# Optimization experiments

Hardware: AMD Instinct MI355X
Metric: run time of the kernel (lower is better)

## Reference

```python
import jax, jax.numpy as jnp
import numpy as np

EPS = 1e-8
VOX_WIDTH = 1.0
CURV_THRESH = 0.5


def _build_kernels():
    """Nine 3x3x3 central finite-difference stencils, pre-divided by vox_width / vox_width^2."""
    def zk():
        return np.zeros((3, 3, 3), np.float32)
    ks = {}
    # first derivatives (central difference), denominator vox_width
    for name, ax in (('ddx', 0), ('ddy', 1), ('ddz', 2)):
        k = zk(); i = [1, 1, 1]
        i[ax] = 0; k[tuple(i)] = -0.5
        i[ax] = 2; k[tuple(i)] = 0.5
        ks[name] = k / VOX_WIDTH
    # pure second derivatives, denominator vox_width^2
    for name, ax in (('d2dx2', 0), ('d2dy2', 1), ('d2dz2', 2)):
        k = zk(); i = [1, 1, 1]
        i[ax] = 0; k[tuple(i)] = 1.0
        i[ax] = 1; k[tuple(i)] = -2.0
        i[ax] = 2; k[tuple(i)] = 1.0
        ks[name] = k / VOX_WIDTH ** 2
    # mixed second derivatives, denominator vox_width^2
    for name, (a, b) in (('d2dxdy', (0, 1)), ('d2dxdz', (0, 2)), ('d2dydz', (1, 2))):
        k = zk()
        for sa, sb, v in ((0, 0, 0.25), (0, 2, -0.25), (2, 0, -0.25), (2, 2, 0.25)):
            i = [1, 1, 1]; i[a] = sa; i[b] = sb; k[tuple(i)] = v
        ks[name] = k / VOX_WIDTH ** 2
    order = ['ddx', 'ddy', 'ddz', 'd2dx2', 'd2dy2', 'd2dz2', 'd2dxdy', 'd2dxdz', 'd2dydz']
    return np.stack([ks[n] for n in order])[:, None]  # [9, 1, 3, 3, 3]


_KERNELS = jnp.asarray(_build_kernels())


def setup_inputs() -> dict:
    key = jax.random.key(0)
    phi = jax.random.normal(key, (2, 1, 192, 192, 192), dtype=jnp.float32)
    return {"phi": phi}


def reference(phi):
    # all nine stencils as one valid 3D conv: [N, 9, D-2, H-2, W-2]
    g = jax.lax.conv_general_dilated(
        phi, _KERNELS, window_strides=(1, 1, 1), padding='VALID',
        dimension_numbers=('NCDHW', 'OIDHW', 'NCDHW'))
    gx, gy, gz, hxx, hyy, hzz, hxy, hxz, hyz = (g[:, i:i + 1] for i in range(9))

    mag = jnp.sqrt(gx * gx + gy * gy + gz * gz + EPS)
    mag3 = mag ** 3

    # mean curvature: sum_{i!=j} g_i^2 H_jj - 2 sum_{i<j} g_i g_j H_ij, over |grad|^3
    cross = gx * gy * hxy + gx * gz * hxz + gy * gz * hyz
    mean_c = (gx * gx * (hyy + hzz) + gy * gy * (hxx + hzz) + gz * gz * (hxx + hyy)
              - 2.0 * cross) / (mag3 + EPS)

    # gaussian curvature: laplacian/|grad| - (g^T H g)/|grad|^3
    lap = (hxx + hyy + hzz) / (mag + EPS)
    quad = (gx * gx * hxx + gy * gy * hyy + gz * gz * hzz + 2.0 * cross) / (mag3 + EPS)
    gauss = lap - quad

    k1 = mean_c + jnp.sqrt(jnp.abs(mean_c ** 2 - gauss) + EPS)
    pen = jax.nn.relu((k1 / (CURV_THRESH + EPS)) ** 2 - 1.0)

    # zero crossings of phi over 3x3x3 neighborhoods (valid -> matches conv output shape)
    mn = jax.lax.reduce_window(phi, jnp.inf, jax.lax.min, (1, 1, 3, 3, 3), (1, 1, 1, 1, 1), 'VALID')
    mx = jax.lax.reduce_window(phi, -jnp.inf, jax.lax.max, (1, 1, 3, 3, 3), (1, 1, 1, 1, 1), 'VALID')
    phi_zero = jax.lax.stop_gradient((mn * mx < 0).astype(phi.dtype))

    return jnp.sum(phi_zero * pen) / (jnp.sum(phi_zero) + EPS)
```

## Files before the change

### kernel.cpp

```cpp
#include <hip/hip_runtime.h>


typedef float v2f __attribute__((ext_vector_type(2)));

constexpr int DIM  = 192;
constexpr int ODIM = 190;
constexpr int TX = 32, TY = 32, CZ = 19;
constexpr int NTX = 6, NTY = 6, NTZ = 10;
constexpr int PLANE = DIM * DIM;
constexpr int NBLOCKS = 2 * NTZ * NTY * NTX;

struct Row { v2f A, B, C; };
struct Slice {
    Row   r[3];
    float xmn[4], xmx[4];
};

#define PREF(T4, T2, g) do {                                             \
    const float* base_ = pn + (zbase + (g)) * PLANE;                     \
    _Pragma("unroll")                                                    \
    for (int dy = 0; dy < 3; ++dy) {                                     \
        T4[dy] = *(const float4*)(base_ + yoff[dy] + c4);                \
        T2[dy] = *(const float2*)(base_ + yoff[dy] + c2);                \
    } } while (0)

#define UNPACK(S, T4, T2) do {                                           \
    float mn6[6], mx6[6];                                                \
    _Pragma("unroll")                                                    \
    for (int dy = 0; dy < 3; ++dy) {                                     \
        const float4 a = T4[dy]; const float2 b = T2[dy];                \
        (S).r[dy].A = (v2f){a.x, a.z};                                   \
        (S).r[dy].B = (v2f){a.y, a.w};                                   \
        (S).r[dy].C = (v2f){b.x, b.y};                                   \
        if (dy == 0) {                                                   \
            mn6[0] = a.x; mn6[1] = a.y; mn6[2] = a.z;                    \
            mn6[3] = a.w; mn6[4] = b.x; mn6[5] = b.y;                    \
            mx6[0] = a.x; mx6[1] = a.y; mx6[2] = a.z;                    \
            mx6[3] = a.w; mx6[4] = b.x; mx6[5] = b.y;                    \
        } else {                                                         \
            mn6[0] = fminf(mn6[0], a.x); mx6[0] = fmaxf(mx6[0], a.x);    \
            mn6[1] = fminf(mn6[1], a.y); mx6[1] = fmaxf(mx6[1], a.y);    \
            mn6[2] = fminf(mn6[2], a.z); mx6[2] = fmaxf(mx6[2], a.z);    \
            mn6[3] = fminf(mn6[3], a.w); mx6[3] = fmaxf(mx6[3], a.w);    \
            mn6[4] = fminf(mn6[4], b.x); mx6[4] = fmaxf(mx6[4], b.x);    \
            mn6[5] = fminf(mn6[5], b.y); mx6[5] = fmaxf(mx6[5], b.y);    \
        }                                                                \
    }                                                                    \
    _Pragma("unroll")                                                    \
    for (int j = 0; j < 4; ++j) {                                        \
        (S).xmn[j] = fminf(fminf(mn6[j], mn6[j + 1]), mn6[j + 2]);       \
        (S).xmx[j] = fmaxf(fmaxf(mx6[j], mx6[j + 1]), mx6[j + 2]);       \
    } } while (0)

__global__ __launch_bounds__(256, 3) void curv_main(const float* __restrict__ phi,
                                                    double* __restrict__ acc,
                                                    float* __restrict__ out,
                                                    unsigned* __restrict__ ticket,
                                                    int mode) {
    int bx = blockIdx.x;
    const int tx = bx % NTX; bx /= NTX;
    const int ty = bx % NTY; bx /= NTY;
    const int tz = bx % NTZ; bx /= NTZ;
    const int n  = bx;

    const int xbase = tx * TX, ybase = ty * TY, zbase = tz * CZ;
    const int tid = threadIdx.x;
    const int row = tid >> 3;
    const int x0  = (tid & 7) * 4;
    const float* pn = phi + (long long)n * DIM * PLANE;

    const int c4 = xbase + x0;
    int c2t = c4 + 4; if (c2t > DIM - 2) c2t = DIM - 2;
    const int c2 = c2t;
    int yoff[3];
#pragma unroll
    for (int dy = 0; dy < 3; ++dy) {
        int iy = ybase + row + dy; if (iy > DIM - 1) iy = DIM - 1;
        yoff[dy] = iy * DIM;
    }

    float4 tA4[3]; float2 tA2[3];
    float4 tB4[3]; float2 tB2[3];

    float fsp = 0.0f, fsc = 0.0f;
    const float EPSF = 1e-8f;
    const float EPS4 = 4e-8f;
    const int oy = ybase + row;

    bool vmask[4];
#pragma unroll
    for (int j = 0; j < 4; ++j)
        vmask[j] = (oy < ODIM) && (xbase + x0 + j < ODIM);

    auto PK = [](const Row& w, int k) -> v2f {
        return k == 0 ? w.A
             : (k == 1 ? w.B
             : (k == 2 ? (v2f){w.A.y, w.C.x}
                       : (v2f){w.B.y, w.C.y}));
    };

    auto compute = [&](const Slice& s0, const Slice& s1, const Slice& s2) {
        float wmn[4], wmx[4];
#pragma unroll
        for (int j = 0; j < 4; ++j) {
            wmn[j] = fminf(fminf(s0.xmn[j], s1.xmn[j]), s2.xmn[j]);
            wmx[j] = fmaxf(fmaxf(s0.xmx[j], s1.xmx[j]), s2.xmx[j]);
        }

#pragma unroll
        for (int p = 0; p < 2; ++p) {
            const v2f a0 = PK(s0.r[1], p + 1);
            const v2f a2 = PK(s2.r[1], p + 1);
            const v2f b0 = PK(s1.r[0], p + 1);
            const v2f b2 = PK(s1.r[2], p + 1);
            const v2f cc = PK(s1.r[1], p + 1);
            const v2f zm = PK(s1.r[1], p);
            const v2f zp = PK(s1.r[1], p + 2);

            v2f Gx = a2 - a0;
            v2f Gy = b2 - b0;
            v2f Gz = zp - zm;

            v2f c2v = 2.0f * cc;
            v2f hxx = a0 - c2v + a2;
            v2f hyy = b0 - c2v + b2;
            v2f hzz = zm - c2v + zp;

            v2f Mxy = PK(s0.r[0], p + 1) - PK(s0.r[2], p + 1)
                    - PK(s2.r[0], p + 1) + PK(s2.r[2], p + 1);
            v2f Mxz = PK(s0.r[1], p) - PK(s0.r[1], p + 2)
                    - PK(s2.r[1], p) + PK(s2.r[1], p + 2);
            v2f Myz = PK(s1.r[0], p) - PK(s1.r[0], p + 2)
                    - PK(s1.r[2], p) + PK(s1.r[2], p + 2);

            v2f Gx2 = Gx * Gx, Gy2 = Gy * Gy, Gz2 = Gz * Gz;
            v2f mag2G = Gx2 + Gy2 + Gz2 + EPS4;

            v2f r = (v2f){ __builtin_amdgcn_rsqf(mag2G.x),
                           __builtin_amdgcn_rsqf(mag2G.y) };
            v2f r3 = r * r * r;
            v2f twor3 = r3 + r3;

            v2f crossG = Gx * Gy * Mxy + Gx * Gz * Mxz + Gy * Gz * Myz;

            v2f num1 = Gx2 * (hyy + hzz) + Gy2 * (hxx + hzz) +
                       Gz2 * (hxx + hyy) - 0.5f * crossG;
            v2f mean_c = num1 * twor3;
            v2f lap   = (hxx + hyy + hzz) * (r + r);
            v2f num2  = Gx2 * hxx + Gy2 * hyy + Gz2 * hzz + 0.5f * crossG;
            v2f quad  = num2 * twor3;
            v2f gauss = lap - quad;

            v2f disc = mean_c * mean_c - gauss;
            v2f sq = (v2f){ sqrtf(fabsf(disc.x) + EPSF),
                            sqrtf(fabsf(disc.y) + EPSF) };
            v2f k1 = mean_c + sq;
            v2f t  = 2.0f * k1;
            v2f pen2 = t * t - 1.0f;

#pragma unroll
            for (int e = 0; e < 2; ++e) {
                const int j = p + 2 * e;
                float pen = fmaxf(e ? pen2.y : pen2.x, 0.0f);
                if (vmask[j] && (wmn[j] * wmx[j] < 0.0f)) {
                    fsp += pen;
                    fsc += 1.0f;
                }
            }
        }
    };

    Slice s0, s1, s2;

    PREF(tA4, tA2, 0); PREF(tB4, tB2, 1);
    UNPACK(s0, tA4, tA2); PREF(tA4, tA2, 2);
    UNPACK(s1, tB4, tB2); PREF(tB4, tB2, 3);

    UNPACK(s2, tA4, tA2); PREF(tA4, tA2, 4);  compute(s0, s1, s2);
    UNPACK(s0, tB4, tB2); PREF(tB4, tB2, 5);  compute(s1, s2, s0);
    UNPACK(s1, tA4, tA2); PREF(tA4, tA2, 6);  compute(s2, s0, s1);
    UNPACK(s2, tB4, tB2); PREF(tB4, tB2, 7);  compute(s0, s1, s2);
    UNPACK(s0, tA4, tA2); PREF(tA4, tA2, 8);  compute(s1, s2, s0);
    UNPACK(s1, tB4, tB2); PREF(tB4, tB2, 9);  compute(s2, s0, s1);
    UNPACK(s2, tA4, tA2); PREF(tA4, tA2, 10); compute(s0, s1, s2);
    UNPACK(s0, tB4, tB2); PREF(tB4, tB2, 11); compute(s1, s2, s0);
    UNPACK(s1, tA4, tA2); PREF(tA4, tA2, 12); compute(s2, s0, s1);
    UNPACK(s2, tB4, tB2); PREF(tB4, tB2, 13); compute(s0, s1, s2);
    UNPACK(s0, tA4, tA2); PREF(tA4, tA2, 14); compute(s1, s2, s0);
    UNPACK(s1, tB4, tB2); PREF(tB4, tB2, 15); compute(s2, s0, s1);
    UNPACK(s2, tA4, tA2); PREF(tA4, tA2, 16); compute(s0, s1, s2);
    UNPACK(s0, tB4, tB2); PREF(tB4, tB2, 17); compute(s1, s2, s0);
    UNPACK(s1, tA4, tA2); PREF(tA4, tA2, 18); compute(s2, s0, s1);
    UNPACK(s2, tB4, tB2); PREF(tB4, tB2, 19); compute(s0, s1, s2);
    UNPACK(s0, tA4, tA2); PREF(tA4, tA2, 20); compute(s1, s2, s0);
    UNPACK(s1, tB4, tB2);                     compute(s2, s0, s1);
    UNPACK(s2, tA4, tA2);                     compute(s0, s1, s2);

    double sp = (double)fsp, sc = (double)fsc;
#pragma unroll
    for (int off = 32; off > 0; off >>= 1) {
        sp += __shfl_down(sp, off, 64);
        sc += __shfl_down(sc, off, 64);
    }

    __shared__ double lsp[4], lsc[4];
    __shared__ int is_last;
    const int wave = tid >> 6, lane = tid & 63;
    if (lane == 0) { lsp[wave] = sp; lsc[wave] = sc; }
    __syncthreads();
    if (tid == 0) {
        double tp = lsp[0] + lsp[1] + lsp[2] + lsp[3];
        double tc = lsc[0] + lsc[1] + lsc[2] + lsc[3];
        if (mode) {
            acc[2 * blockIdx.x]     = tp;
            acc[2 * blockIdx.x + 1] = tc;
            __threadfence();
            unsigned prev = atomicAdd(ticket, 1u);
            is_last = (prev == (unsigned)(NBLOCKS - 1)) ? 1 : 0;
        } else {
            atomicAdd(&acc[0], tp);
            atomicAdd(&acc[1], tc);
            is_last = 0;
        }
    }
    __syncthreads();

    if (is_last) {
        __threadfence();
        double rp = 0.0, rc = 0.0;
        for (int i = tid; i < NBLOCKS; i += 256) {
            rp += acc[2 * i];
            rc += acc[2 * i + 1];
        }
#pragma unroll
        for (int off = 32; off > 0; off >>= 1) {
            rp += __shfl_down(rp, off, 64);
            rc += __shfl_down(rc, off, 64);
        }
        if (lane == 0) { lsp[wave] = rp; lsc[wave] = rc; }
        __syncthreads();
        if (tid == 0) {
            double tp = lsp[0] + lsp[1] + lsp[2] + lsp[3];
            double tc = lsc[0] + lsc[1] + lsc[2] + lsc[3];
            out[0] = (float)(tp / (tc + 1e-8));
        }
    }
}

__global__ void curv_reduce(const double* __restrict__ acc,
                            float* __restrict__ out) {
    if (threadIdx.x == 0)
        out[0] = (float)(acc[0] / (acc[1] + 1e-8));
}

extern "C" void kernel_launch(void* const* d_in, const int* in_sizes, int n_in,
                              void* d_out, int out_size, void* d_ws, size_t ws_size,
                              hipStream_t stream) {
    const float* phi = (const float*)d_in[0];
    float* out = (float*)d_out;
    double* acc = (double*)d_ws;

    const size_t need = (size_t)(2 * NBLOCKS) * sizeof(double) + sizeof(unsigned);
    if (ws_size >= need) {
        unsigned* ticket = (unsigned*)(acc + 2 * NBLOCKS);
        hipMemsetAsync(ticket, 0, sizeof(unsigned), stream);
        curv_main<<<NBLOCKS, 256, 0, stream>>>(phi, acc, out, ticket, 1);
    } else {
        hipMemsetAsync(d_ws, 0, 2 * sizeof(double), stream);
        curv_main<<<NBLOCKS, 256, 0, stream>>>(phi, acc, out, (unsigned*)nullptr, 0);
        curv_reduce<<<1, 256, 0, stream>>>(acc, out);
    }
}
```

Measured before the change: 121.7 us.

## Precompute shifted pair vectors and replace last-block ticket reduction with a separate reduce kernel

Each slice now stores four pre-packed v2f windows per row, including the two shifted pairs, so the stencil code indexes them directly instead of building them per use. The fused last-block reduction, with its ticket memset, atomic ticket and thread fences, is replaced by plain per-block partial writes followed by a separate one-block reduce kernel. This removes the memset and the fence/atomic tail from the main kernel, at the cost of an extra kernel launch and slightly more register state per slice.

```diff
diff --git a/kernel.cpp b/kernel.cpp
--- a/kernel.cpp
+++ b/kernel.cpp
@@ -10,9 +10,8 @@
 constexpr int PLANE = DIM * DIM;
 constexpr int NBLOCKS = 2 * NTZ * NTY * NTX;
 
-struct Row { v2f A, B, C; };
 struct Slice {
-    Row   r[3];
+    v2f   q[3][4];
     float xmn[4], xmx[4];
 };
 
@@ -29,9 +28,10 @@
     _Pragma("unroll")                                                    \
     for (int dy = 0; dy < 3; ++dy) {                                     \
         const float4 a = T4[dy]; const float2 b = T2[dy];                \
-        (S).r[dy].A = (v2f){a.x, a.z};                                   \
-        (S).r[dy].B = (v2f){a.y, a.w};                                   \
-        (S).r[dy].C = (v2f){b.x, b.y};                                   \
+        (S).q[dy][0] = (v2f){a.x, a.z};                                  \
+        (S).q[dy][1] = (v2f){a.y, a.w};                                  \
+        (S).q[dy][2] = (v2f){a.z, b.x};                                  \
+        (S).q[dy][3] = (v2f){a.w, b.y};                                  \
         if (dy == 0) {                                                   \
             mn6[0] = a.x; mn6[1] = a.y; mn6[2] = a.z;                    \
             mn6[3] = a.w; mn6[4] = b.x; mn6[5] = b.y;                    \
@@ -54,9 +54,7 @@
 
 __global__ __launch_bounds__(256, 3) void curv_main(const float* __restrict__ phi,
                                                     double* __restrict__ acc,
-                                                    float* __restrict__ out,
-                                                    unsigned* __restrict__ ticket,
-                                                    int mode) {
+                                                    int use_partials) {
     int bx = blockIdx.x;
     const int tx = bx % NTX; bx /= NTX;
     const int ty = bx % NTY; bx /= NTY;
@@ -92,13 +90,6 @@
     for (int j = 0; j < 4; ++j)
         vmask[j] = (oy < ODIM) && (xbase + x0 + j < ODIM);
 
-    auto PK = [](const Row& w, int k) -> v2f {
-        return k == 0 ? w.A
-             : (k == 1 ? w.B
-             : (k == 2 ? (v2f){w.A.y, w.C.x}
-                       : (v2f){w.B.y, w.C.y}));
-    };
-
     auto compute = [&](const Slice& s0, const Slice& s1, const Slice& s2) {
         float wmn[4], wmx[4];
 #pragma unroll
@@ -109,29 +100,21 @@
 
 #pragma unroll
         for (int p = 0; p < 2; ++p) {
-            const v2f a0 = PK(s0.r[1], p + 1);
-            const v2f a2 = PK(s2.r[1], p + 1);
-            const v2f b0 = PK(s1.r[0], p + 1);
-            const v2f b2 = PK(s1.r[2], p + 1);
-            const v2f cc = PK(s1.r[1], p + 1);
-            const v2f zm = PK(s1.r[1], p);
-            const v2f zp = PK(s1.r[1], p + 2);
-
-            v2f Gx = a2 - a0;
-            v2f Gy = b2 - b0;
-            v2f Gz = zp - zm;
-
-            v2f c2v = 2.0f * cc;
-            v2f hxx = a0 - c2v + a2;
-            v2f hyy = b0 - c2v + b2;
-            v2f hzz = zm - c2v + zp;
-
-            v2f Mxy = PK(s0.r[0], p + 1) - PK(s0.r[2], p + 1)
-                    - PK(s2.r[0], p + 1) + PK(s2.r[2], p + 1);
-            v2f Mxz = PK(s0.r[1], p) - PK(s0.r[1], p + 2)
-                    - PK(s2.r[1], p) + PK(s2.r[1], p + 2);
-            v2f Myz = PK(s1.r[0], p) - PK(s1.r[0], p + 2)
-                    - PK(s1.r[2], p) + PK(s1.r[2], p + 2);
+            v2f Gx = s2.q[1][p + 1] - s0.q[1][p + 1];
+            v2f Gy = s1.q[2][p + 1] - s1.q[0][p + 1];
+            v2f Gz = s1.q[1][p + 2] - s1.q[1][p];
+
+            v2f c2v = 2.0f * s1.q[1][p + 1];
+            v2f hxx = s0.q[1][p + 1] - c2v + s2.q[1][p + 1];
+            v2f hyy = s1.q[0][p + 1] - c2v + s1.q[2][p + 1];
+            v2f hzz = s1.q[1][p] - c2v + s1.q[1][p + 2];
+
+            v2f Mxy = s0.q[0][p + 1] - s0.q[2][p + 1]
+                    - s2.q[0][p + 1] + s2.q[2][p + 1];
+            v2f Mxz = s0.q[1][p] - s0.q[1][p + 2]
+                    - s2.q[1][p] + s2.q[1][p + 2];
+            v2f Myz = s1.q[0][p] - s1.q[0][p + 2]
+                    - s1.q[2][p] + s1.q[2][p + 2];
 
             v2f Gx2 = Gx * Gx, Gy2 = Gy * Gy, Gz2 = Gz * Gz;
             v2f mag2G = Gx2 + Gy2 + Gz2 + EPS4;
@@ -204,53 +187,48 @@
     }
 
     __shared__ double lsp[4], lsc[4];
-    __shared__ int is_last;
     const int wave = tid >> 6, lane = tid & 63;
     if (lane == 0) { lsp[wave] = sp; lsc[wave] = sc; }
     __syncthreads();
     if (tid == 0) {
         double tp = lsp[0] + lsp[1] + lsp[2] + lsp[3];
         double tc = lsc[0] + lsc[1] + lsc[2] + lsc[3];
-        if (mode) {
+        if (use_partials) {
             acc[2 * blockIdx.x]     = tp;
             acc[2 * blockIdx.x + 1] = tc;
-            __threadfence();
-            unsigned prev = atomicAdd(ticket, 1u);
-            is_last = (prev == (unsigned)(NBLOCKS - 1)) ? 1 : 0;
         } else {
             atomicAdd(&acc[0], tp);
             atomicAdd(&acc[1], tc);
-            is_last = 0;
-        }
-    }
+        }
+    }
+}
+
+__global__ __launch_bounds__(256) void curv_reduce(const double* __restrict__ part,
+                                                   int nblocks, int use_partials,
+                                                   float* __restrict__ out) {
+    double sp = 0.0, sc = 0.0;
+    if (use_partials) {
+        for (int i = threadIdx.x; i < nblocks; i += 256) {
+            sp += part[2 * i];
+            sc += part[2 * i + 1];
+        }
+    } else if (threadIdx.x == 0) {
+        sp = part[0]; sc = part[1];
+    }
+#pragma unroll
+    for (int off = 32; off > 0; off >>= 1) {
+        sp += __shfl_down(sp, off, 64);
+        sc += __shfl_down(sc, off, 64);
+    }
+    __shared__ double lsp[4], lsc[4];
+    const int wave = threadIdx.x >> 6, lane = threadIdx.x & 63;
+    if (lane == 0) { lsp[wave] = sp; lsc[wave] = sc; }
     __syncthreads();
-
-    if (is_last) {
-        __threadfence();
-        double rp = 0.0, rc = 0.0;
-        for (int i = tid; i < NBLOCKS; i += 256) {
-            rp += acc[2 * i];
-            rc += acc[2 * i + 1];
-        }
-#pragma unroll
-        for (int off = 32; off > 0; off >>= 1) {
-            rp += __shfl_down(rp, off, 64);
-            rc += __shfl_down(rc, off, 64);
-        }
-        if (lane == 0) { lsp[wave] = rp; lsc[wave] = rc; }
-        __syncthreads();
-        if (tid == 0) {
-            double tp = lsp[0] + lsp[1] + lsp[2] + lsp[3];
-            double tc = lsc[0] + lsc[1] + lsc[2] + lsc[3];
-            out[0] = (float)(tp / (tc + 1e-8));
-        }
-    }
-}
-
-__global__ void curv_reduce(const double* __restrict__ acc,
-                            float* __restrict__ out) {
-    if (threadIdx.x == 0)
-        out[0] = (float)(acc[0] / (acc[1] + 1e-8));
+    if (threadIdx.x == 0) {
+        double tp = lsp[0] + lsp[1] + lsp[2] + lsp[3];
+        double tc = lsc[0] + lsc[1] + lsc[2] + lsc[3];
+        out[0] = (float)(tp / (tc + 1e-8));
+    }
 }
 
 extern "C" void kernel_launch(void* const* d_in, const int* in_sizes, int n_in,
@@ -260,14 +238,11 @@
     float* out = (float*)d_out;
     double* acc = (double*)d_ws;
 
-    const size_t need = (size_t)(2 * NBLOCKS) * sizeof(double) + sizeof(unsigned);
-    if (ws_size >= need) {
-        unsigned* ticket = (unsigned*)(acc + 2 * NBLOCKS);
-        hipMemsetAsync(ticket, 0, sizeof(unsigned), stream);
-        curv_main<<<NBLOCKS, 256, 0, stream>>>(phi, acc, out, ticket, 1);
-    } else {
+    const int use_partials = (ws_size >= (size_t)(2 * NBLOCKS) * sizeof(double)) ? 1 : 0;
+    if (!use_partials) {
         hipMemsetAsync(d_ws, 0, 2 * sizeof(double), stream);
-        curv_main<<<NBLOCKS, 256, 0, stream>>>(phi, acc, out, (unsigned*)nullptr, 0);
-        curv_reduce<<<1, 256, 0, stream>>>(acc, out);
-    }
+    }
+
+    curv_main<<<NBLOCKS, 256, 0, stream>>>(phi, acc, use_partials);
+    curv_reduce<<<1, 256, 0, stream>>>(acc, NBLOCKS, use_partials, out);
 }
```

New measurement: 110.1 us. -9.5%, faster.
